# Performance work log

Measured on AMD Instinct MI355X. Metric: run time of the kernel, lower is better.

The kernel has to match this reference:

```python
import jax, jax.numpy as jnp
import numpy as np

N_NODES = 50000
N_EDGES = 800000
D_FEAT = 128
HIDDEN = 128
OUT = 64
HEADS = 4


def setup_inputs() -> dict:
    key = jax.random.key(0)
    ks = jax.random.split(key, 12)
    s_in = 1.0 / np.sqrt(D_FEAT)
    s_h = 1.0 / np.sqrt(HIDDEN)
    x = jax.random.normal(ks[0], (N_NODES, D_FEAT), dtype=jnp.float32)
    edge_index = jax.random.randint(ks[1], (2, N_EDGES), 0, N_NODES, dtype=jnp.int32)
    return {
        "x": x,
        "edge_index": edge_index,
        # SAGEConv params: lin_l (aggregated neighbors), lin_r (root), bias
        "W_l": jax.random.normal(ks[2], (D_FEAT, HIDDEN), dtype=jnp.float32) * s_in,
        "W_r": jax.random.normal(ks[3], (D_FEAT, HIDDEN), dtype=jnp.float32) * s_in,
        "b_sage": jnp.zeros((HIDDEN,), dtype=jnp.float32),
        # GATConv params: lin_src, lin_dst (heads*hidden each), att vectors, bias
        "W_src": jax.random.normal(ks[4], (HIDDEN, HEADS * HIDDEN), dtype=jnp.float32) * s_h,
        "W_dst": jax.random.normal(ks[5], (HIDDEN, HEADS * HIDDEN), dtype=jnp.float32) * s_h,
        "att_src": jax.random.normal(ks[6], (HEADS, HIDDEN), dtype=jnp.float32) * s_h,
        "att_dst": jax.random.normal(ks[7], (HEADS, HIDDEN), dtype=jnp.float32) * s_h,
        "b_gat": jnp.zeros((HIDDEN,), dtype=jnp.float32),
        # Final Linear
        "W_lin": jax.random.normal(ks[8], (HIDDEN, OUT), dtype=jnp.float32) * s_h,
        "b_lin": jnp.zeros((OUT,), dtype=jnp.float32),
    }


def reference(x, edge_index, W_l, W_r, b_sage, W_src, W_dst, att_src, att_dst, b_gat, W_lin, b_lin):
    N = x.shape[0]
    src = edge_index[0]
    dst = edge_index[1]

    # ---- SAGEConv (mean aggregation): out = lin_l(mean_j x_j) + lin_r(x_i) + b ----
    agg = jax.ops.segment_sum(x[src], dst, num_segments=N)          # [N, d]
    cnt = jax.ops.segment_sum(jnp.ones_like(dst, dtype=x.dtype), dst, num_segments=N)
    mean_nbr = agg / jnp.maximum(cnt, 1.0)[:, None]
    h = mean_nbr @ W_l + x @ W_r + b_sage                           # [N, H*... no: [N, hidden]
    h = jax.nn.relu(h)

    # ---- GATConv (heads=4, concat=False -> mean over heads) ----
    H, C = att_src.shape
    hs = (h @ W_src).reshape(N, H, C)                               # source-transformed [N, H, C]
    hd = (h @ W_dst).reshape(N, H, C)                               # dest-transformed   [N, H, C]
    a_s = jnp.einsum('nhc,hc->nh', hs, att_src)                     # [N, H]
    a_d = jnp.einsum('nhc,hc->nh', hd, att_dst)                     # [N, H]
    e = jax.nn.leaky_relu(a_s[src] + a_d[dst], negative_slope=0.2)  # [E, H]
    # edge softmax over incoming edges per destination node
    e_max = jax.ops.segment_max(e, dst, num_segments=N)             # [N, H]
    e_exp = jnp.exp(e - e_max[dst])                                 # [E, H]
    denom = jax.ops.segment_sum(e_exp, dst, num_segments=N)         # [N, H]
    alpha = e_exp / denom[dst]                                      # [E, H]
    msg = hs[src] * alpha[:, :, None]                               # [E, H, C]
    out = jax.ops.segment_sum(msg, dst, num_segments=N)             # [N, H, C]
    out = out.mean(axis=1) + b_gat                                  # concat=False: avg heads
    out = jax.nn.relu(out)

    # ---- final Linear ----
    return out @ W_lin + b_lin
```

## Files before the change

kernel.cpp:

```cpp
#include <hip/hip_runtime.h>

#define D 128
#define HEADS 4

typedef __attribute__((ext_vector_type(8))) short short8;
typedef __attribute__((ext_vector_type(4))) float f32x4;
typedef __attribute__((ext_vector_type(2))) float f32x2;

static __device__ __forceinline__ float leaky(float v) { return v > 0.f ? v : 0.2f * v; }

static __device__ __forceinline__ f32x2 bf2_to_p2(unsigned int u) {
    union { unsigned int i; float f; } a, b;
    a.i = u << 16;
    b.i = u & 0xffff0000u;
    f32x2 r; r.x = a.f; r.y = b.f;
    return r;
}
static __device__ __forceinline__ float bf_to_f(unsigned short s) {
    union { unsigned int i; float f; } a;
    a.i = ((unsigned int)s) << 16;
    return a.f;
}
static __device__ __forceinline__ unsigned short f2bf(float f) {
    union { float f; unsigned int i; } v; v.f = f;
    unsigned int u = v.i;
    unsigned int r = (u + 0x7fffu + ((u >> 16) & 1u)) >> 16;
    return (unsigned short)r;
}

static __device__ __forceinline__ void pk_fma(f32x2& acc, f32x2 v, f32x2 w) {
    asm("v_pk_fma_f32 %0, %1, %2, %0" : "+v"(acc) : "v"(v), "v"(w));
}
static __device__ __forceinline__ void pk_fma_lo(f32x2& acc, f32x2 v, f32x2 w) {
    asm("v_pk_fma_f32 %0, %1, %2, %0 op_sel:[0,0,0] op_sel_hi:[1,0,1]"
        : "+v"(acc) : "v"(v), "v"(w));
}
static __device__ __forceinline__ void pk_fma_hi(f32x2& acc, f32x2 v, f32x2 w) {
    asm("v_pk_fma_f32 %0, %1, %2, %0 op_sel:[0,1,0] op_sel_hi:[1,1,1]"
        : "+v"(acc) : "v"(v), "v"(w));
}
static __device__ __forceinline__ void pk_add(f32x2& acc, f32x2 v) {
    asm("v_pk_add_f32 %0, %1, %0" : "+v"(acc) : "v"(v));
}

#define CPAD 16
#define PREP_CNT 107520
#define MAXBUCK 2048
#define BSLOT 1024
#define CH 8192

__global__ __launch_bounds__(256) void k_early(const float* __restrict__ x, int npairs,
                                               const int* __restrict__ ei, int E, int nbuck, int scatB,
                                               int* __restrict__ bcur,
                                               unsigned int* __restrict__ ebuf,
                                               const float* __restrict__ Wl, const float* __restrict__ Wr,
                                               const float* __restrict__ Wsrc, const float* __restrict__ Wlin,
                                               const float* __restrict__ Wdst,
                                               const float* __restrict__ atts, const float* __restrict__ attd,
                                               unsigned short* __restrict__ Bh,
                                               unsigned short* __restrict__ Bg,
                                               unsigned short* __restrict__ Bf,
                                               float* __restrict__ wsd,
                                               unsigned int* __restrict__ xb) {
    __shared__ unsigned int sval[CH];
    __shared__ unsigned short soff[CH];
    __shared__ int cnt[MAXBUCK];
    __shared__ int gbase[MAXBUCK];
    int gb = blockIdx.x, t = threadIdx.x;
    if (gb < scatB) {
        int c0 = gb * CH;
        int ecnt = E - c0; if (ecnt > CH) ecnt = CH;
        for (int i = t; i < MAXBUCK; i += 256) cnt[i] = 0;
        __syncthreads();
        for (int i = t; i < ecnt; i += 256) {
            int s = ei[c0 + i], d = ei[E + c0 + i];
            int b = d >> 5;
            soff[i] = (unsigned short)atomicAdd(&cnt[b], 1);
            sval[i] = (unsigned int)s | ((unsigned int)(d & 31) << 16) | ((unsigned int)b << 21);
        }
        __syncthreads();
        for (int b = t; b < nbuck; b += 256)
            if (cnt[b]) gbase[b] = (b << 10) + atomicAdd(&bcur[b * CPAD], cnt[b]);
        __syncthreads();
        for (int i = t; i < ecnt; i += 256) {
            unsigned int v = sval[i];
            int b = v >> 21;
            int pos = gbase[b] + soff[i];
            if (pos < ((b + 1) << 10)) ebuf[pos] = v & 0x1fffffu;
        }
        return;
    }
    int i = (gb - scatB) * 256 + t;
    if (i < 32768) {
        int idx = i;
        int j = idx & 7, n16 = (idx >> 3) & 15, quad = (idx >> 7) & 3, rest = idx >> 9;
        int nc = rest & 7, kb = rest >> 3;
        int kk = kb * 32 + quad * 8 + j;
        int n = nc * 16 + n16;
        float v = (kk < 128) ? Wl[kk * 128 + n] : Wr[(kk - 128) * 128 + n];
        Bh[idx] = f2bf(v);
    } else if (i < 32768 + 65536) {
        int idx = i - 32768;
        int j = idx & 7, n16 = (idx >> 3) & 15, quad = (idx >> 7) & 3, rest = idx >> 9;
        int nc = rest & 7, kb = rest >> 3;
        int kk = kb * 32 + quad * 8 + j;
        int n = nc * 16 + n16;
        float v = Wsrc[(kk & 127) * 512 + (kk >> 7) * 128 + n];
        Bg[idx] = f2bf(v);
    } else if (i < 32768 + 65536 + 8192) {
        int idx = i - 98304;
        int j = idx & 7, n16 = (idx >> 3) & 15, quad = (idx >> 7) & 3, rest = idx >> 9;
        int nc = rest & 3, kb = rest >> 2;
        int kk = kb * 32 + quad * 8 + j;
        int n = nc * 16 + n16;
        Bf[idx] = f2bf(Wlin[kk * 64 + n]);
    } else if (i < PREP_CNT) {
        int tt = i - 106496;
        int k = tt >> 3, o = tt & 7;
        int hh = o & 3;
        const float* W = (o < 4) ? Wsrc : Wdst;
        const float* att = (o < 4) ? atts : attd;
        float acc = 0.f;
        for (int c = 0; c < 128; c++) acc += W[k * 512 + hh * 128 + c] * att[hh * 128 + c];
        wsd[o * 132 + k] = acc;
    } else {
        int p = i - PREP_CNT;
        if (p < npairs) {
            float2 v = *(const float2*)(x + (size_t)p * 2);
            xb[p] = (unsigned int)f2bf(v.x) | ((unsigned int)f2bf(v.y) << 16);
        }
    }
}

#define BCAP 1024
__global__ __launch_bounds__(256) void k_build_sage(const unsigned int* __restrict__ ebuf,
                                                    const int* __restrict__ bcur,
                                                    const unsigned int* __restrict__ xb,
                                                    int* __restrict__ csr,
                                                    int* __restrict__ rowptr,
                                                    int* __restrict__ rowend,
                                                    unsigned int* __restrict__ meanb, int N) {
    __shared__ int cnt[32];
    __shared__ int excl[33];
    __shared__ unsigned char off[BCAP];
    __shared__ unsigned int rawv[BCAP];
    __shared__ int sorted[BCAP];
    int b = blockIdx.x, t = threadIdx.x;
    int e0 = b << 10;
    int ecnt = bcur[b * CPAD];
    if (ecnt > BCAP) ecnt = BCAP;
    if (t < 32) cnt[t] = 0;
    __syncthreads();
    for (int i = t; i < ecnt; i += 256) {
        unsigned int p = ebuf[e0 + i];
        rawv[i] = p;
        off[i] = (unsigned char)atomicAdd(&cnt[(p >> 16) & 31], 1);
    }
    __syncthreads();
    if (t == 0) {
        int run = 0;
        #pragma unroll
        for (int j = 0; j < 32; j++) { excl[j] = run; run += cnt[j]; }
        excl[32] = run;
    }
    __syncthreads();
    for (int i = t; i < ecnt; i += 256) {
        unsigned int p = rawv[i];
        int d = (p >> 16) & 31;
        sorted[excl[d] + off[i]] = (int)((p & 0xffffu) << 6);
    }
    __syncthreads();
    int nb0 = b << 5;
    if (t < 32 && nb0 + t < N) {
        rowptr[nb0 + t] = e0 + excl[t];
        rowend[nb0 + t] = e0 + excl[t + 1];
    }
    for (int i = t; i < ecnt; i += 256) csr[e0 + i] = sorted[i];
    int wv = t >> 6, lane = t & 63;
    for (int k = 0; k < 8; k++) {
        int local = wv * 8 + k;
        int node = nb0 + local;
        if (node >= N) continue;
        int le0 = excl[local], le1 = excl[local + 1];
        f32x2 aA = {0.f, 0.f}, aB = {0.f, 0.f};
        int e = le0;
        for (; e + 3 < le1; e += 4) {
            int s0 = sorted[e], s1 = sorted[e + 1], s2 = sorted[e + 2], s3 = sorted[e + 3];
            unsigned int u0 = xb[(unsigned)(s0 + lane)];
            unsigned int u1 = xb[(unsigned)(s1 + lane)];
            unsigned int u2 = xb[(unsigned)(s2 + lane)];
            unsigned int u3 = xb[(unsigned)(s3 + lane)];
            pk_add(aA, bf2_to_p2(u0));
            pk_add(aB, bf2_to_p2(u1));
            pk_add(aA, bf2_to_p2(u2));
            pk_add(aB, bf2_to_p2(u3));
        }
        for (; e < le1; e++)
            pk_add(aA, bf2_to_p2(xb[(unsigned)(sorted[e] + lane)]));
        pk_add(aA, aB);
        int dg = le1 - le0;
        float inv = 1.0f / (float)(dg > 0 ? dg : 1);
        unsigned int o = (unsigned int)f2bf(aA.x * inv) | ((unsigned int)f2bf(aA.y * inv) << 16);
        __builtin_nontemporal_store(o, meanb + (size_t)node * 64 + lane);
    }
}

__global__ __launch_bounds__(256) void k_mfma_h(const unsigned short* __restrict__ A0,
                                                const unsigned short* __restrict__ A1,
                                                const unsigned short* __restrict__ Bp,
                                                const float* __restrict__ bias,
                                                const float* __restrict__ wsd,
                                                unsigned short* __restrict__ outb,
                                                float* __restrict__ a_s,
                                                float* __restrict__ a_d, int M) {
    const int NC = 8;
    __shared__ unsigned short sH[64][136];
    __shared__ float swsd[1056];
    int tid = threadIdx.x;
    int wave = tid >> 6;
    int lane = tid & 63;
    int row0 = blockIdx.x * 64 + wave * 16;
    int n16 = lane & 15, quad = lane >> 4;
    int arow = row0 + n16;
    int arowc = arow < M ? arow : 0;
    for (int i = tid; i < 1056; i += 256) swsd[i] = wsd[i];
    f32x4 acc[NC];
    #pragma unroll
    for (int i = 0; i < NC; i++) acc[i] = (f32x4){0.f, 0.f, 0.f, 0.f};
    #pragma unroll
    for (int kb = 0; kb < 8; kb++) {
        const unsigned short* ap = (kb < 4)
            ? (A0 + (size_t)arowc * 128 + kb * 32 + quad * 8)
            : (A1 + (size_t)arowc * 128 + (kb - 4) * 32 + quad * 8);
        short8 af = *(const short8*)ap;
        #pragma unroll
        for (int nc = 0; nc < NC; nc++) {
            short8 bf = *(const short8*)(Bp + ((((size_t)(kb * NC + nc) * 4 + quad) * 16 + n16) << 3));
            acc[nc] = __builtin_amdgcn_mfma_f32_16x16x32_bf16(af, bf, acc[nc], 0, 0, 0);
        }
    }
    int orow = row0 + quad * 4;
    int lrow = wave * 16 + quad * 4;
    #pragma unroll
    for (int r = 0; r < 4; r++) {
        int m = orow + r;
        #pragma unroll
        for (int nc = 0; nc < NC; nc++) {
            int col = nc * 16 + n16;
            float v = fmaxf(acc[nc][r] + bias[col], 0.f);
            unsigned short bv = f2bf(v);
            sH[lrow + r][col] = bv;
            if (m < M) outb[(size_t)m * 128 + col] = bv;
        }
    }
    __syncthreads();
    #pragma unroll
    for (int j = tid; j < 512; j += 256) {
        int m = j >> 3, o = j & 7;
        const float* wr = swsd + o * 132;
        f32x2 pa = {0.f, 0.f}, pb = {0.f, 0.f};
        #pragma unroll 4
        for (int kb = 0; kb < 16; kb++) {
            const unsigned int* hp = (const unsigned int*)&sH[m][kb * 8];
            unsigned int h0 = hp[0], h1 = hp[1], h2 = hp[2], h3 = hp[3];
            f32x4 wa = *(const f32x4*)(wr + kb * 8);
            f32x4 wb = *(const f32x4*)(wr + kb * 8 + 4);
            pk_fma(pa, bf2_to_p2(h0), __builtin_shufflevector(wa, wa, 0, 1));
            pk_fma(pb, bf2_to_p2(h1), __builtin_shufflevector(wa, wa, 2, 3));
            pk_fma(pa, bf2_to_p2(h2), __builtin_shufflevector(wb, wb, 0, 1));
            pk_fma(pb, bf2_to_p2(h3), __builtin_shufflevector(wb, wb, 2, 3));
        }
        pk_add(pa, pb);
        float accd = pa.x + pa.y;
        int n = blockIdx.x * 64 + m;
        if (n < M) {
            if (o < 4) a_s[n * 4 + o] = accd;
            else       a_d[n * 4 + (o - 4)] = accd;
        }
    }
}

#define EDGE_CAP 192
__global__ __launch_bounds__(256) void k_gat_agg(const int* __restrict__ rowptr,
                                                 const int* __restrict__ rowend,
                                                 const int* __restrict__ csr,
                                                 const unsigned int* __restrict__ hb,
                                                 const float* __restrict__ a_s,
                                                 const float* __restrict__ a_d,
                                                 unsigned int* __restrict__ aggb, int N) {
    __shared__ int   sSrc[4][EDGE_CAP];
    __shared__ float sAl[4][EDGE_CAP * 4];
    int wv = threadIdx.x >> 6;
    int lane = threadIdx.x & 63;
    int n = blockIdx.x * 4 + wv;
    bool active = n < N;
    int e0 = 0, deg = 0;
    float4 ad = {0.f, 0.f, 0.f, 0.f};
    if (active) {
        e0 = rowptr[n];
        deg = rowend[n] - e0;
        ad = *(const float4*)(a_d + (size_t)n * 4);
    }
    f32x4 psum = {0.f, 0.f, 0.f, 0.f};
    for (int base = 0; base < deg; base += 64) {
        int i = base + lane;
        if (i < deg) {
            int s64 = csr[e0 + i];
            float4 as = *(const float4*)(a_s + (size_t)(s64 >> 4));
            f32x4 w;
            w.x = __expf(leaky(as.x + ad.x));
            w.y = __expf(leaky(as.y + ad.y));
            w.z = __expf(leaky(as.z + ad.z));
            w.w = __expf(leaky(as.w + ad.w));
            psum += w;
            if (i < EDGE_CAP) {
                sSrc[wv][i] = s64;
                *(f32x4*)&sAl[wv][i * 4] = w;
            }
        }
    }
    #pragma unroll
    for (int o = 32; o; o >>= 1) {
        psum.x += __shfl_xor(psum.x, o);
        psum.y += __shfl_xor(psum.y, o);
        psum.z += __shfl_xor(psum.z, o);
        psum.w += __shfl_xor(psum.w, o);
    }
    f32x4 inv;
    inv.x = psum.x > 0.f ? 0.25f / psum.x : 0.f;
    inv.y = psum.y > 0.f ? 0.25f / psum.y : 0.f;
    inv.z = psum.z > 0.f ? 0.25f / psum.z : 0.f;
    inv.w = psum.w > 0.f ? 0.25f / psum.w : 0.f;
    int capdeg = deg < EDGE_CAP ? deg : EDGE_CAP;
    for (int base = 0; base < capdeg; base += 64) {
        int i = base + lane;
        if (i < capdeg) {
            f32x4 w = *(f32x4*)&sAl[wv][i * 4];
            w *= inv;
            *(f32x4*)&sAl[wv][i * 4] = w;
        }
    }
    __syncthreads();
    f32x2 ac0 = {0.f, 0.f}, ac1 = {0.f, 0.f}, ac2 = {0.f, 0.f}, ac3 = {0.f, 0.f};
    int e = 0;
    for (; e + 3 < capdeg; e += 4) {
        int o0 = sSrc[wv][e], o1 = sSrc[wv][e + 1], o2 = sSrc[wv][e + 2], o3 = sSrc[wv][e + 3];
        f32x4 w0 = *(const f32x4*)&sAl[wv][e * 4];
        f32x4 w1 = *(const f32x4*)&sAl[wv][e * 4 + 4];
        f32x4 w2 = *(const f32x4*)&sAl[wv][e * 4 + 8];
        f32x4 w3 = *(const f32x4*)&sAl[wv][e * 4 + 12];
        unsigned int u0 = hb[(unsigned)(o0 + lane)];
        unsigned int u1 = hb[(unsigned)(o1 + lane)];
        unsigned int u2 = hb[(unsigned)(o2 + lane)];
        unsigned int u3 = hb[(unsigned)(o3 + lane)];
        f32x2 v0 = bf2_to_p2(u0), v1 = bf2_to_p2(u1), v2 = bf2_to_p2(u2), v3 = bf2_to_p2(u3);
        f32x2 w0a = __builtin_shufflevector(w0, w0, 0, 1), w0b = __builtin_shufflevector(w0, w0, 2, 3);
        f32x2 w1a = __builtin_shufflevector(w1, w1, 0, 1), w1b = __builtin_shufflevector(w1, w1, 2, 3);
        f32x2 w2a = __builtin_shufflevector(w2, w2, 0, 1), w2b = __builtin_shufflevector(w2, w2, 2, 3);
        f32x2 w3a = __builtin_shufflevector(w3, w3, 0, 1), w3b = __builtin_shufflevector(w3, w3, 2, 3);
        pk_fma_lo(ac0, v0, w0a); pk_fma_hi(ac1, v0, w0a); pk_fma_lo(ac2, v0, w0b); pk_fma_hi(ac3, v0, w0b);
        pk_fma_lo(ac0, v1, w1a); pk_fma_hi(ac1, v1, w1a); pk_fma_lo(ac2, v1, w1b); pk_fma_hi(ac3, v1, w1b);
        pk_fma_lo(ac0, v2, w2a); pk_fma_hi(ac1, v2, w2a); pk_fma_lo(ac2, v2, w2b); pk_fma_hi(ac3, v2, w2b);
        pk_fma_lo(ac0, v3, w3a); pk_fma_hi(ac1, v3, w3a); pk_fma_lo(ac2, v3, w3b); pk_fma_hi(ac3, v3, w3b);
    }
    for (; e < capdeg; e++) {
        int o0 = sSrc[wv][e];
        f32x4 w0 = *(const f32x4*)&sAl[wv][e * 4];
        f32x2 v0 = bf2_to_p2(hb[(unsigned)(o0 + lane)]);
        f32x2 wa = __builtin_shufflevector(w0, w0, 0, 1), wb = __builtin_shufflevector(w0, w0, 2, 3);
        pk_fma_lo(ac0, v0, wa); pk_fma_hi(ac1, v0, wa);
        pk_fma_lo(ac2, v0, wb); pk_fma_hi(ac3, v0, wb);
    }
    for (int i = EDGE_CAP; i < deg; i++) {
        int s64 = csr[e0 + i];
        float4 as = *(const float4*)(a_s + (size_t)(s64 >> 4));
        f32x4 w;
        w.x = __expf(leaky(as.x + ad.x)) * inv.x;
        w.y = __expf(leaky(as.y + ad.y)) * inv.y;
        w.z = __expf(leaky(as.z + ad.z)) * inv.z;
        w.w = __expf(leaky(as.w + ad.w)) * inv.w;
        f32x2 v0 = bf2_to_p2(hb[(unsigned)(s64 + lane)]);
        f32x2 wa = __builtin_shufflevector(w, w, 0, 1), wb = __builtin_shufflevector(w, w, 2, 3);
        pk_fma_lo(ac0, v0, wa); pk_fma_hi(ac1, v0, wa);
        pk_fma_lo(ac2, v0, wb); pk_fma_hi(ac3, v0, wb);
    }
    if (!active) return;
    unsigned int* rowu = aggb + (size_t)n * 256 + lane;
    unsigned int o0 = (unsigned int)f2bf(ac0.x) | ((unsigned int)f2bf(ac0.y) << 16);
    unsigned int o1 = (unsigned int)f2bf(ac1.x) | ((unsigned int)f2bf(ac1.y) << 16);
    unsigned int o2 = (unsigned int)f2bf(ac2.x) | ((unsigned int)f2bf(ac2.y) << 16);
    unsigned int o3 = (unsigned int)f2bf(ac3.x) | ((unsigned int)f2bf(ac3.y) << 16);
    __builtin_nontemporal_store(o0, rowu + 0);
    __builtin_nontemporal_store(o1, rowu + 64);
    __builtin_nontemporal_store(o2, rowu + 128);
    __builtin_nontemporal_store(o3, rowu + 192);
}

__global__ __launch_bounds__(256) void k_mfma_tail(const unsigned short* __restrict__ aggb,
                                                   const unsigned short* __restrict__ Bg,
                                                   const float* __restrict__ bg,
                                                   const unsigned short* __restrict__ Bf,
                                                   const float* __restrict__ bl,
                                                   float* __restrict__ out, int M) {
    __shared__ unsigned short sG[64][136];
    int wave = threadIdx.x >> 6;
    int lane = threadIdx.x & 63;
    int row0 = blockIdx.x * 64 + wave * 16;
    int n16 = lane & 15, quad = lane >> 4;
    {
        int arow = row0 + n16;
        int arowc = arow < M ? arow : 0;
        const unsigned short* ap = aggb + (size_t)arowc * 512 + quad * 8;
        f32x4 acc[8];
        #pragma unroll
        for (int i = 0; i < 8; i++) acc[i] = (f32x4){0.f, 0.f, 0.f, 0.f};
        #pragma unroll
        for (int kb = 0; kb < 16; kb++) {
            short8 af = *(const short8*)(ap + kb * 32);
            #pragma unroll
            for (int nc = 0; nc < 8; nc++) {
                short8 bf = *(const short8*)(Bg + ((((size_t)(kb * 8 + nc) * 4 + quad) * 16 + n16) << 3));
                acc[nc] = __builtin_amdgcn_mfma_f32_16x16x32_bf16(af, bf, acc[nc], 0, 0, 0);
            }
        }
        int lrow = wave * 16 + quad * 4;
        #pragma unroll
        for (int r = 0; r < 4; r++) {
            #pragma unroll
            for (int nc = 0; nc < 8; nc++) {
                int col = nc * 16 + n16;
                sG[lrow + r][col] = f2bf(fmaxf(acc[nc][r] + bg[col], 0.f));
            }
        }
    }
    __syncthreads();
    {
        f32x4 acc[4];
        #pragma unroll
        for (int i = 0; i < 4; i++) acc[i] = (f32x4){0.f, 0.f, 0.f, 0.f};
        #pragma unroll
        for (int kb = 0; kb < 4; kb++) {
            short8 af = *(const short8*)&sG[wave * 16 + n16][kb * 32 + quad * 8];
            #pragma unroll
            for (int nc = 0; nc < 4; nc++) {
                short8 bf = *(const short8*)(Bf + ((((size_t)(kb * 4 + nc) * 4 + quad) * 16 + n16) << 3));
                acc[nc] = __builtin_amdgcn_mfma_f32_16x16x32_bf16(af, bf, acc[nc], 0, 0, 0);
            }
        }
        int orow = row0 + quad * 4;
        #pragma unroll
        for (int r = 0; r < 4; r++) {
            int m = orow + r;
            if (m < M) {
                #pragma unroll
                for (int nc = 0; nc < 4; nc++) {
                    int col = nc * 16 + n16;
                    out[(size_t)m * 64 + col] = acc[nc][r] + bl[col];
                }
            }
        }
    }
}

extern "C" void kernel_launch(void* const* d_in, const int* in_sizes, int n_in,
                              void* d_out, int out_size, void* d_ws, size_t ws_size,
                              hipStream_t stream) {
    const float* x    = (const float*)d_in[0];
    const int*   ei   = (const int*)d_in[1];
    const float* Wl   = (const float*)d_in[2];
    const float* Wr   = (const float*)d_in[3];
    const float* bs   = (const float*)d_in[4];
    const float* Wsrc = (const float*)d_in[5];
    const float* Wdst = (const float*)d_in[6];
    const float* atts = (const float*)d_in[7];
    const float* attd = (const float*)d_in[8];
    const float* bg   = (const float*)d_in[9];
    const float* Wlin = (const float*)d_in[10];
    const float* bl   = (const float*)d_in[11];
    int N = in_sizes[0] / D;
    int E = in_sizes[1] / 2;
    int nbuck = (N + 31) >> 5;
    int npairs = N * 64;

    char* w = (char*)d_ws;
    auto alloc = [&](size_t bytes) {
        char* p = w;
        w += (bytes + 255) & ~(size_t)255;
        return p;
    };
    unsigned int* xb     = (unsigned int*)alloc((size_t)N * 256);
    unsigned int* meanb  = (unsigned int*)alloc((size_t)N * 256);
    unsigned int* hb     = (unsigned int*)alloc((size_t)N * 256);
    unsigned int* aggb   = (unsigned int*)alloc((size_t)N * 1024);
    unsigned short* Bh   = (unsigned short*)alloc(65536 * 2);
    unsigned short* Bg   = (unsigned short*)alloc(65536 * 2);
    unsigned short* Bf   = (unsigned short*)alloc(8192 * 2);
    float* a_s           = (float*)alloc((size_t)N * 16);
    float* a_d           = (float*)alloc((size_t)N * 16);
    float* wsd           = (float*)alloc(1056 * 4);
    int* rowptr          = (int*)alloc((size_t)N * 4);
    int* rowend          = (int*)alloc((size_t)N * 4);
    int* bcur            = (int*)alloc((size_t)MAXBUCK * CPAD * 4);
    unsigned int* ebuf   = (unsigned int*)alloc((size_t)MAXBUCK * BSLOT * 4);
    int* csr             = (int*)alloc((size_t)MAXBUCK * BSLOT * 4);
    (void)ws_size; (void)n_in; (void)out_size;

    hipMemsetAsync(bcur, 0, (size_t)MAXBUCK * CPAD * 4, stream);

    int scatB = (E + CH - 1) / CH;
    int workBlocks = (PREP_CNT + npairs + 255) / 256;
    k_early<<<scatB + workBlocks, 256, 0, stream>>>(x, npairs, ei, E, nbuck, scatB,
                                                    bcur, ebuf,
                                                    Wl, Wr, Wsrc, Wlin, Wdst, atts, attd,
                                                    Bh, Bg, Bf, wsd, xb);
    k_build_sage<<<nbuck, 256, 0, stream>>>(ebuf, bcur, xb, csr, rowptr, rowend, meanb, N);

    k_mfma_h<<<(N + 63) / 64, 256, 0, stream>>>((const unsigned short*)meanb,
                                                (const unsigned short*)xb, Bh, bs, wsd,
                                                (unsigned short*)hb, a_s, a_d, N);
    k_gat_agg<<<(N + 3) / 4, 256, 0, stream>>>(rowptr, rowend, csr, hb, a_s, a_d, aggb, N);
    k_mfma_tail<<<(N + 63) / 64, 256, 0, stream>>>((const unsigned short*)aggb, Bg, bg,
                                                   Bf, bl, (float*)d_out, N);
}
```

Baseline: 240.4 us.

## Split waves into half-wave edge pairs with 8-byte loads and software-pipelined gathers

Both the SAGE mean aggregation and the GAT aggregation now have each half-wave handle a different edge, with every lane loading 8 bytes instead of 4. Gathers are double-buffered in groups of 8 edges so loads for the next group are issued before the current group is accumulated, and the two halves are combined with a cross-half shuffle at the end. EDGE_CAP drops from 192 to 64, which shrinks shared memory and may raise occupancy, but edges beyond 64 now take the slow uncached path that recomputes exp per edge. The split also adds shuffle reductions and masked padding work for short rows.

```diff
diff --git a/kernel.cpp b/kernel.cpp
--- a/kernel.cpp
+++ b/kernel.cpp
@@ -6,6 +6,7 @@
 typedef __attribute__((ext_vector_type(8))) short short8;
 typedef __attribute__((ext_vector_type(4))) float f32x4;
 typedef __attribute__((ext_vector_type(2))) float f32x2;
+typedef __attribute__((ext_vector_type(2))) unsigned int u32x2;
 
 static __device__ __forceinline__ float leaky(float v) { return v > 0.f ? v : 0.2f * v; }
 
@@ -16,16 +17,14 @@
     f32x2 r; r.x = a.f; r.y = b.f;
     return r;
 }
-static __device__ __forceinline__ float bf_to_f(unsigned short s) {
-    union { unsigned int i; float f; } a;
-    a.i = ((unsigned int)s) << 16;
-    return a.f;
-}
 static __device__ __forceinline__ unsigned short f2bf(float f) {
     union { float f; unsigned int i; } v; v.f = f;
     unsigned int u = v.i;
     unsigned int r = (u + 0x7fffu + ((u >> 16) & 1u)) >> 16;
     return (unsigned short)r;
+}
+static __device__ __forceinline__ unsigned int packbf(f32x2 v) {
+    return (unsigned int)f2bf(v.x) | ((unsigned int)f2bf(v.y) << 16);
 }
 
 static __device__ __forceinline__ void pk_fma(f32x2& acc, f32x2 v, f32x2 w) {
@@ -177,31 +176,58 @@
     }
     for (int i = t; i < ecnt; i += 256) csr[e0 + i] = sorted[i];
     int wv = t >> 6, lane = t & 63;
+    int c2 = (lane & 31) << 1;
+    int hf = lane >> 5;
     for (int k = 0; k < 8; k++) {
         int local = wv * 8 + k;
         int node = nb0 + local;
         if (node >= N) continue;
         int le0 = excl[local], le1 = excl[local + 1];
+        int dg = le1 - le0;
         f32x2 aA = {0.f, 0.f}, aB = {0.f, 0.f};
-        int e = le0;
-        for (; e + 3 < le1; e += 4) {
-            int s0 = sorted[e], s1 = sorted[e + 1], s2 = sorted[e + 2], s3 = sorted[e + 3];
-            unsigned int u0 = xb[(unsigned)(s0 + lane)];
-            unsigned int u1 = xb[(unsigned)(s1 + lane)];
-            unsigned int u2 = xb[(unsigned)(s2 + lane)];
-            unsigned int u3 = xb[(unsigned)(s3 + lane)];
-            pk_add(aA, bf2_to_p2(u0));
-            pk_add(aB, bf2_to_p2(u1));
-            pk_add(aA, bf2_to_p2(u2));
-            pk_add(aB, bf2_to_p2(u3));
-        }
-        for (; e < le1; e++)
-            pk_add(aA, bf2_to_p2(xb[(unsigned)(sorted[e] + lane)]));
-        pk_add(aA, aB);
-        int dg = le1 - le0;
-        float inv = 1.0f / (float)(dg > 0 ? dg : 1);
-        unsigned int o = (unsigned int)f2bf(aA.x * inv) | ((unsigned int)f2bf(aA.y * inv) << 16);
-        __builtin_nontemporal_store(o, meanb + (size_t)node * 64 + lane);
+        if (dg > 0) {
+            u32x2 u0[4], u1[4];
+            auto ld = [&](int base, u32x2* uu) {
+                #pragma unroll
+                for (int j = 0; j < 4; j++) {
+                    int idx = base + 2 * j + hf;
+                    int s64 = sorted[idx < le1 ? idx : le0];
+                    uu[j] = *(const u32x2*)(xb + (unsigned)(s64 + c2));
+                }
+            };
+            auto acc = [&](int base, u32x2* uu) {
+                #pragma unroll
+                for (int j = 0; j < 4; j++) {
+                    int idx = base + 2 * j + hf;
+                    u32x2 u = uu[j];
+                    if (idx >= le1) { u[0] = 0u; u[1] = 0u; }
+                    pk_add(aA, bf2_to_p2(u[0]));
+                    pk_add(aB, bf2_to_p2(u[1]));
+                }
+            };
+            ld(le0, u0);
+            int bb = le0 + 8;
+            for (; bb < le1; bb += 8) {
+                ld(bb, u1);
+                acc(bb - 8, u0);
+                #pragma unroll
+                for (int j = 0; j < 4; j++) u0[j] = u1[j];
+            }
+            acc(bb - 8, u0);
+        }
+        aA.x += __shfl_xor(aA.x, 32);
+        aA.y += __shfl_xor(aA.y, 32);
+        aB.x += __shfl_xor(aB.x, 32);
+        aB.y += __shfl_xor(aB.y, 32);
+        if (lane < 32) {
+            float inv = 1.0f / (float)(dg > 0 ? dg : 1);
+            u32x2 o;
+            f32x2 sa = aA; sa.x *= inv; sa.y *= inv;
+            f32x2 sb = aB; sb.x *= inv; sb.y *= inv;
+            o[0] = packbf(sa);
+            o[1] = packbf(sb);
+            __builtin_nontemporal_store(o, (u32x2*)(meanb + (size_t)node * 64 + c2));
+        }
     }
 }
 
@@ -280,7 +306,7 @@
     }
 }
 
-#define EDGE_CAP 192
+#define EDGE_CAP 64
 __global__ __launch_bounds__(256) void k_gat_agg(const int* __restrict__ rowptr,
                                                  const int* __restrict__ rowend,
                                                  const int* __restrict__ csr,
@@ -332,44 +358,54 @@
     inv.z = psum.z > 0.f ? 0.25f / psum.z : 0.f;
     inv.w = psum.w > 0.f ? 0.25f / psum.w : 0.f;
     int capdeg = deg < EDGE_CAP ? deg : EDGE_CAP;
-    for (int base = 0; base < capdeg; base += 64) {
-        int i = base + lane;
+    {
+        int i = lane;
         if (i < capdeg) {
             f32x4 w = *(f32x4*)&sAl[wv][i * 4];
             w *= inv;
             *(f32x4*)&sAl[wv][i * 4] = w;
         }
     }
-    __syncthreads();
-    f32x2 ac0 = {0.f, 0.f}, ac1 = {0.f, 0.f}, ac2 = {0.f, 0.f}, ac3 = {0.f, 0.f};
-    int e = 0;
-    for (; e + 3 < capdeg; e += 4) {
-        int o0 = sSrc[wv][e], o1 = sSrc[wv][e + 1], o2 = sSrc[wv][e + 2], o3 = sSrc[wv][e + 3];
-        f32x4 w0 = *(const f32x4*)&sAl[wv][e * 4];
-        f32x4 w1 = *(const f32x4*)&sAl[wv][e * 4 + 4];
-        f32x4 w2 = *(const f32x4*)&sAl[wv][e * 4 + 8];
-        f32x4 w3 = *(const f32x4*)&sAl[wv][e * 4 + 12];
-        unsigned int u0 = hb[(unsigned)(o0 + lane)];
-        unsigned int u1 = hb[(unsigned)(o1 + lane)];
-        unsigned int u2 = hb[(unsigned)(o2 + lane)];
-        unsigned int u3 = hb[(unsigned)(o3 + lane)];
-        f32x2 v0 = bf2_to_p2(u0), v1 = bf2_to_p2(u1), v2 = bf2_to_p2(u2), v3 = bf2_to_p2(u3);
-        f32x2 w0a = __builtin_shufflevector(w0, w0, 0, 1), w0b = __builtin_shufflevector(w0, w0, 2, 3);
-        f32x2 w1a = __builtin_shufflevector(w1, w1, 0, 1), w1b = __builtin_shufflevector(w1, w1, 2, 3);
-        f32x2 w2a = __builtin_shufflevector(w2, w2, 0, 1), w2b = __builtin_shufflevector(w2, w2, 2, 3);
-        f32x2 w3a = __builtin_shufflevector(w3, w3, 0, 1), w3b = __builtin_shufflevector(w3, w3, 2, 3);
-        pk_fma_lo(ac0, v0, w0a); pk_fma_hi(ac1, v0, w0a); pk_fma_lo(ac2, v0, w0b); pk_fma_hi(ac3, v0, w0b);
-        pk_fma_lo(ac0, v1, w1a); pk_fma_hi(ac1, v1, w1a); pk_fma_lo(ac2, v1, w1b); pk_fma_hi(ac3, v1, w1b);
-        pk_fma_lo(ac0, v2, w2a); pk_fma_hi(ac1, v2, w2a); pk_fma_lo(ac2, v2, w2b); pk_fma_hi(ac3, v2, w2b);
-        pk_fma_lo(ac0, v3, w3a); pk_fma_hi(ac1, v3, w3a); pk_fma_lo(ac2, v3, w3b); pk_fma_hi(ac3, v3, w3b);
-    }
-    for (; e < capdeg; e++) {
-        int o0 = sSrc[wv][e];
-        f32x4 w0 = *(const f32x4*)&sAl[wv][e * 4];
-        f32x2 v0 = bf2_to_p2(hb[(unsigned)(o0 + lane)]);
-        f32x2 wa = __builtin_shufflevector(w0, w0, 0, 1), wb = __builtin_shufflevector(w0, w0, 2, 3);
-        pk_fma_lo(ac0, v0, wa); pk_fma_hi(ac1, v0, wa);
-        pk_fma_lo(ac2, v0, wb); pk_fma_hi(ac3, v0, wb);
+    int c2 = (lane & 31) << 1;
+    int hf = lane >> 5;
+    f32x2 a0l = {0.f,0.f}, a0h = {0.f,0.f}, a1l = {0.f,0.f}, a1h = {0.f,0.f};
+    f32x2 a2l = {0.f,0.f}, a2h = {0.f,0.f}, a3l = {0.f,0.f}, a3h = {0.f,0.f};
+    if (capdeg > 0) {
+        u32x2 u0[4], u1[4];
+        auto ld = [&](int base, u32x2* uu) {
+            #pragma unroll
+            for (int j = 0; j < 4; j++) {
+                int idx = base + 2 * j + hf;
+                int s64 = sSrc[wv][idx < capdeg ? idx : 0];
+                uu[j] = *(const u32x2*)(hb + (unsigned)(s64 + c2));
+            }
+        };
+        auto cons = [&](int base, u32x2* uu) {
+            #pragma unroll
+            for (int j = 0; j < 4; j++) {
+                int idx = base + 2 * j + hf;
+                u32x2 u = uu[j];
+                if (idx >= capdeg) { u[0] = 0u; u[1] = 0u; }
+                const f32x4 w4 = *(const f32x4*)&sAl[wv][(idx < capdeg ? idx : 0) * 4];
+                f32x2 wa = __builtin_shufflevector(w4, w4, 0, 1);
+                f32x2 wb = __builtin_shufflevector(w4, w4, 2, 3);
+                f32x2 p0 = bf2_to_p2(u[0]);
+                f32x2 p1 = bf2_to_p2(u[1]);
+                pk_fma_lo(a0l, p0, wa); pk_fma_lo(a0h, p1, wa);
+                pk_fma_hi(a1l, p0, wa); pk_fma_hi(a1h, p1, wa);
+                pk_fma_lo(a2l, p0, wb); pk_fma_lo(a2h, p1, wb);
+                pk_fma_hi(a3l, p0, wb); pk_fma_hi(a3h, p1, wb);
+            }
+        };
+        ld(0, u0);
+        int bb = 8;
+        for (; bb < capdeg; bb += 8) {
+            ld(bb, u1);
+            cons(bb - 8, u0);
+            #pragma unroll
+            for (int j = 0; j < 4; j++) u0[j] = u1[j];
+        }
+        cons(bb - 8, u0);
     }
     for (int i = EDGE_CAP; i < deg; i++) {
         int s64 = csr[e0 + i];
@@ -379,21 +415,39 @@
         w.y = __expf(leaky(as.y + ad.y)) * inv.y;
         w.z = __expf(leaky(as.z + ad.z)) * inv.z;
         w.w = __expf(leaky(as.w + ad.w)) * inv.w;
-        f32x2 v0 = bf2_to_p2(hb[(unsigned)(s64 + lane)]);
-        f32x2 wa = __builtin_shufflevector(w, w, 0, 1), wb = __builtin_shufflevector(w, w, 2, 3);
-        pk_fma_lo(ac0, v0, wa); pk_fma_hi(ac1, v0, wa);
-        pk_fma_lo(ac2, v0, wb); pk_fma_hi(ac3, v0, wb);
+        if (!hf) {
+            u32x2 u = *(const u32x2*)(hb + (unsigned)(s64 + c2));
+            f32x2 p0 = bf2_to_p2(u[0]);
+            f32x2 p1 = bf2_to_p2(u[1]);
+            f32x2 wa = __builtin_shufflevector(w, w, 0, 1);
+            f32x2 wb = __builtin_shufflevector(w, w, 2, 3);
+            pk_fma_lo(a0l, p0, wa); pk_fma_lo(a0h, p1, wa);
+            pk_fma_hi(a1l, p0, wa); pk_fma_hi(a1h, p1, wa);
+            pk_fma_lo(a2l, p0, wb); pk_fma_lo(a2h, p1, wb);
+            pk_fma_hi(a3l, p0, wb); pk_fma_hi(a3h, p1, wb);
+        }
     }
     if (!active) return;
-    unsigned int* rowu = aggb + (size_t)n * 256 + lane;
-    unsigned int o0 = (unsigned int)f2bf(ac0.x) | ((unsigned int)f2bf(ac0.y) << 16);
-    unsigned int o1 = (unsigned int)f2bf(ac1.x) | ((unsigned int)f2bf(ac1.y) << 16);
-    unsigned int o2 = (unsigned int)f2bf(ac2.x) | ((unsigned int)f2bf(ac2.y) << 16);
-    unsigned int o3 = (unsigned int)f2bf(ac3.x) | ((unsigned int)f2bf(ac3.y) << 16);
-    __builtin_nontemporal_store(o0, rowu + 0);
-    __builtin_nontemporal_store(o1, rowu + 64);
-    __builtin_nontemporal_store(o2, rowu + 128);
-    __builtin_nontemporal_store(o3, rowu + 192);
+    a0l.x += __shfl_xor(a0l.x, 32); a0l.y += __shfl_xor(a0l.y, 32);
+    a0h.x += __shfl_xor(a0h.x, 32); a0h.y += __shfl_xor(a0h.y, 32);
+    a1l.x += __shfl_xor(a1l.x, 32); a1l.y += __shfl_xor(a1l.y, 32);
+    a1h.x += __shfl_xor(a1h.x, 32); a1h.y += __shfl_xor(a1h.y, 32);
+    a2l.x += __shfl_xor(a2l.x, 32); a2l.y += __shfl_xor(a2l.y, 32);
+    a2h.x += __shfl_xor(a2h.x, 32); a2h.y += __shfl_xor(a2h.y, 32);
+    a3l.x += __shfl_xor(a3l.x, 32); a3l.y += __shfl_xor(a3l.y, 32);
+    a3h.x += __shfl_xor(a3h.x, 32); a3h.y += __shfl_xor(a3h.y, 32);
+    if (lane < 32) {
+        unsigned int* rowu = aggb + (size_t)n * 256 + c2;
+        u32x2 o;
+        o[0] = packbf(a0l); o[1] = packbf(a0h);
+        __builtin_nontemporal_store(o, (u32x2*)(rowu));
+        o[0] = packbf(a1l); o[1] = packbf(a1h);
+        __builtin_nontemporal_store(o, (u32x2*)(rowu + 64));
+        o[0] = packbf(a2l); o[1] = packbf(a2h);
+        __builtin_nontemporal_store(o, (u32x2*)(rowu + 128));
+        o[0] = packbf(a3l); o[1] = packbf(a3h);
+        __builtin_nontemporal_store(o, (u32x2*)(rowu + 192));
+    }
 }
 
 __global__ __launch_bounds__(256) void k_mfma_tail(const unsigned short* __restrict__ aggb,
```

New measurement: 251.2 us. +4.5%, slower.
